# Kernel tuning notes

Measured on AMD Instinct MI355X. Metric: run time of the kernel, lower is better.

## Reference

```python
import jax, jax.numpy as jnp
import numpy as np

N_NODES = 100000
N_EDGES = 1600000
D = 128
NUM_GRAPHS = 256


def setup_inputs() -> dict:
    key = jax.random.key(0)
    ks = jax.random.split(key, 8)
    x = jax.random.normal(ks[0], (N_NODES, D), dtype=jnp.float32)
    edge_index = jax.random.randint(ks[1], (2, N_EDGES), 0, N_NODES, dtype=jnp.int32)
    edge_attr = jax.random.normal(ks[2], (N_EDGES, D), dtype=jnp.float32) * 0.1
    batch = jnp.sort(jax.random.randint(ks[3], (N_NODES,), 0, NUM_GRAPHS, dtype=jnp.int32))
    primary = jax.random.randint(ks[4], (N_NODES,), 0, 2, dtype=jnp.int32)  # 1=primary, 0=condition
    scale = 1.0 / np.sqrt(D)
    W1 = jax.random.normal(ks[5], (D, D), dtype=jnp.float32) * scale
    b1 = jnp.zeros((D,), dtype=jnp.float32)
    W2 = jax.random.normal(ks[6], (D, D), dtype=jnp.float32) * scale
    b2 = jnp.zeros((D,), dtype=jnp.float32)
    return {"x": x, "edge_index": edge_index, "edge_attr": edge_attr,
            "batch": batch, "primary": primary,
            "W1": W1, "b1": b1, "W2": W2, "b2": b2}


def reference(x, edge_index, edge_attr, batch, primary, W1, b1, W2, b2):
    n = x.shape[0]
    # --- GIN-style GNN layer: node_rep = MLP(x + sum_{e:(s->d)} (x[s] + e_attr)) ---
    src, dst = edge_index[0], edge_index[1]
    msg = x[src] + edge_attr                                  # [E, D] gather (memory-bound)
    agg = jax.ops.segment_sum(msg, dst, num_segments=n)       # [N, D] scatter-add
    h = jax.nn.relu((x + agg) @ W1 + b1) @ W2 + b2            # [N, D]

    # --- per-graph mean pool over condition nodes (primary == 0) ---
    cond = (primary == 0)
    condf = cond.astype(h.dtype)[:, None]
    csum = jax.ops.segment_sum(h * condf, batch, num_segments=NUM_GRAPHS)   # [G, D]
    ccnt = jax.ops.segment_sum(condf, batch, num_segments=NUM_GRAPHS)       # [G, 1]
    # graphs with no condition nodes get a zero pool (matches torch branch)
    pool = jnp.where(ccnt > 0, csum / jnp.maximum(ccnt, 1.0), 0.0)          # [G, D]

    # --- assemble rows: per graph, primary rows [h | cond_pool] first, then zero rows
    # for condition nodes (matches the torch concat order) ---
    key = batch * 2 + cond.astype(batch.dtype)      # primary nodes sort before condition nodes
    order = jnp.argsort(key, stable=True)
    h_o = h[order]                                   # [N, D]
    pool_o = pool[batch[order]]                      # [N, D]
    prim_o = (primary[order] == 1)[:, None]
    out = jnp.where(prim_o, jnp.concatenate([h_o, pool_o], axis=1), 0.0)    # [N, 2D]
    return out
```

## Files before the change

### kernel.cpp

```cpp
#include <hip/hip_runtime.h>

#define D 128
#define NG 256

typedef __attribute__((ext_vector_type(8))) short bf16x8;
typedef __attribute__((ext_vector_type(4))) float f32x4;
typedef __attribute__((ext_vector_type(4))) float f4;
typedef __attribute__((ext_vector_type(4))) ushort u16x4;

__device__ inline ushort f2bf(float f) {
  uint b = __float_as_uint(f);
  return (ushort)((b + 0x7fffu + ((b >> 16) & 1u)) >> 16);
}
__device__ inline float bf2f(ushort u) { return __uint_as_float((uint)u << 16); }

__global__ __launch_bounds__(256) void prep_kernel(
    const int* __restrict__ ei, int* __restrict__ deg,
    const int* __restrict__ batch, const int* __restrict__ primary,
    int* __restrict__ ncount, int* __restrict__ ccnt,
    const float* __restrict__ x, ushort* __restrict__ xb,
    const float* __restrict__ W1, const float* __restrict__ W2,
    ushort* __restrict__ W1T, ushort* __restrict__ W2T, int E, int N, int total4) {
  int i = blockIdx.x * blockDim.x + threadIdx.x;
  if (i < E) atomicAdd(&deg[ei[E + i]], 1);
  if (i < N) {
    int g = batch[i];
    atomicAdd(&ncount[g], 1);
    if (primary[i] == 0) atomicAdd(&ccnt[g], 1);
  }
  if (i < total4) {
    f4 v = __builtin_nontemporal_load(&((const f4*)x)[i]);
    u16x4 o;
    o.x = f2bf(v.x); o.y = f2bf(v.y); o.z = f2bf(v.z); o.w = f2bf(v.w);
    ((u16x4*)xb)[i] = o;
  }
  if (i < 2 * D * D) {
    int w = i >> 14;
    int k = (i >> 7) & 127;
    int n = i & 127;
    const float* src = w ? W2 : W1;
    ushort* dst = w ? W2T : W1T;
    dst[n * 128 + k] = f2bf(src[k * 128 + n]);
  }
}

__global__ __launch_bounds__(256) void scan_block_sums(const int* __restrict__ deg,
                                                       int* __restrict__ bsum, int N) {
  __shared__ int red[256];
  int t = threadIdx.x;
  int base = blockIdx.x * 1024;
  int s = 0;
#pragma unroll
  for (int j = 0; j < 4; ++j) {
    int i = base + t * 4 + j;
    if (i < N) s += deg[i];
  }
  red[t] = s;
  __syncthreads();
  for (int o = 128; o > 0; o >>= 1) {
    if (t < o) red[t] += red[t + o];
    __syncthreads();
  }
  if (t == 0) bsum[blockIdx.x] = red[0];
}

__global__ void scan_bsum(int* __restrict__ bsum, int nb) {
  __shared__ int a[128];
  int t = threadIdx.x;
  int v = (t < nb) ? bsum[t] : 0;
  a[t] = v;
  __syncthreads();
  for (int o = 1; o < 128; o <<= 1) {
    int u = (t >= o) ? a[t - o] : 0;
    __syncthreads();
    a[t] += u;
    __syncthreads();
  }
  if (t < nb) bsum[t] = a[t] - v;
}

__global__ __launch_bounds__(256) void scan_final(const int* __restrict__ deg,
                                                  const int* __restrict__ bsum,
                                                  int* __restrict__ off, int N) {
  __shared__ int ts[256];
  int t = threadIdx.x;
  int base = blockIdx.x * 1024;
  int v[4];
  int s = 0;
#pragma unroll
  for (int j = 0; j < 4; ++j) {
    int i = base + t * 4 + j;
    v[j] = (i < N) ? deg[i] : 0;
    s += v[j];
  }
  ts[t] = s;
  __syncthreads();
  for (int o = 1; o < 256; o <<= 1) {
    int u = (t >= o) ? ts[t - o] : 0;
    __syncthreads();
    ts[t] += u;
    __syncthreads();
  }
  int excl = ts[t] - s + bsum[blockIdx.x];
#pragma unroll
  for (int j = 0; j < 4; ++j) {
    int i = base + t * 4 + j;
    if (i < N) off[i] = excl;
    excl += v[j];
    if (i == N - 1) off[N] = excl;
  }
}

__global__ __launch_bounds__(256, 8) void msg_build_kernel(
    const int* __restrict__ ei, const ushort* __restrict__ xb,
    const float* __restrict__ ea, const int* __restrict__ off,
    int* __restrict__ cursor, ushort* __restrict__ msg, int E) {
  int g = (int)(((long long)blockIdx.x * 256 + threadIdx.x) >> 5);
  int c = threadIdx.x & 31;
  if (g >= E) return;
  int s = ei[g];
  int d = ei[E + g];
  int slot;
  if (c == 0) slot = atomicAdd(&cursor[d], 1);
  slot = __shfl(slot, 0, 32);
  long long row = (long long)off[d] + slot;
  f4 a = __builtin_nontemporal_load(&((const f4*)ea)[(size_t)g * 32 + c]);
  u16x4 u = ((const u16x4*)xb)[(size_t)s * 32 + c];
  u16x4 o;
  o.x = f2bf(a.x + bf2f(u.x));
  o.y = f2bf(a.y + bf2f(u.y));
  o.z = f2bf(a.z + bf2f(u.z));
  o.w = f2bf(a.w + bf2f(u.w));
  __builtin_nontemporal_store(o, &((u16x4*)msg)[(size_t)row * 32 + c]);
}

__global__ void scan_kernel(const int* __restrict__ ncount, int* __restrict__ gstart) {
  __shared__ int a[NG];
  int tx = threadIdx.x;
  int v = ncount[tx];
  a[tx] = v;
  __syncthreads();
  for (int off = 1; off < NG; off <<= 1) {
    int u = (tx >= off) ? a[tx - off] : 0;
    __syncthreads();
    a[tx] += u;
    __syncthreads();
  }
  gstart[tx] = a[tx] - v;
  if (tx == NG - 1) gstart[NG] = a[tx];
}

__global__ __launch_bounds__(256) void rank_kernel(const int* __restrict__ primary,
                                                   const int* __restrict__ gstart,
                                                   const int* __restrict__ ccnt,
                                                   int* __restrict__ pos) {
  int g = blockIdx.x;
  int s = gstart[g], e = gstart[g + 1];
  int pcnt = (e - s) - ccnt[g];
  __shared__ int wcntP[4], wcntC[4];
  int prun = 0, crun = 0;
  for (int i0 = s; i0 < e; i0 += 256) {
    int n = i0 + threadIdx.x;
    bool valid = n < e;
    int isP = (valid && primary[n] == 1) ? 1 : 0;
    int isC = (valid && primary[n] != 1) ? 1 : 0;
    unsigned long long mP = __ballot(isP);
    unsigned long long mC = __ballot(isC);
    int lane = threadIdx.x & 63;
    int wid = threadIdx.x >> 6;
    if (lane == 0) { wcntP[wid] = __popcll(mP); wcntC[wid] = __popcll(mC); }
    __syncthreads();
    int preP = __popcll(mP & ((1ULL << lane) - 1ULL));
    int preC = __popcll(mC & ((1ULL << lane) - 1ULL));
    int woffP = 0, woffC = 0;
#pragma unroll
    for (int ww = 0; ww < 4; ++ww)
      if (ww < wid) { woffP += wcntP[ww]; woffC += wcntC[ww]; }
    int totP = wcntP[0] + wcntP[1] + wcntP[2] + wcntP[3];
    int totC = wcntC[0] + wcntC[1] + wcntC[2] + wcntC[3];
    if (valid) {
      if (isP)
        pos[n] = s + prun + woffP + preP;
      else
        pos[n] = ~(s + pcnt + crun + woffC + preC);
    }
    prun += totP;
    crun += totC;
    __syncthreads();
  }
}

__global__ __launch_bounds__(256, 4) void fused_reduce_mlp_kernel(
    const ushort* __restrict__ xb, const ushort* __restrict__ msg,
    const int* __restrict__ off, float* __restrict__ out,
    const ushort* __restrict__ W1T, const float* __restrict__ b1,
    const ushort* __restrict__ W2T, const float* __restrict__ b2,
    const int* __restrict__ batch, const int* __restrict__ primary,
    const int* __restrict__ pos, float* __restrict__ csum, int N) {
  __shared__ ushort ylds[64][D];
  __shared__ ushort tl[4][16][D];
  __shared__ float csl[4][D];
  const int tid = threadIdx.x;
  const int base = blockIdx.x * 64;

  for (int i = tid; i < 4 * D; i += 256) ((float*)csl)[i] = 0.f;
  const int gmin = batch[base < N ? base : N - 1];

  {
    const int gid = tid >> 5;
    const int c = tid & 31;
    const u16x4* msg4 = (const u16x4*)msg;
    const u16x4* xb4 = (const u16x4*)xb;
    for (int i = 0; i < 8; ++i) {
      const int m = gid * 8 + i;
      const int n = base + m;
      f4 acc = {0.f, 0.f, 0.f, 0.f};
      if (n < N) {
        u16x4 self = xb4[(size_t)n * 32 + c];
        acc.x = bf2f(self.x);
        acc.y = bf2f(self.y);
        acc.z = bf2f(self.z);
        acc.w = bf2f(self.w);
        int k = off[n];
        const int e = off[n + 1];
        for (; k + 4 <= e; k += 4) {
          u16x4 u0 = msg4[(size_t)k * 32 + c];
          u16x4 u1 = msg4[(size_t)(k + 1) * 32 + c];
          u16x4 u2 = msg4[(size_t)(k + 2) * 32 + c];
          u16x4 u3 = msg4[(size_t)(k + 3) * 32 + c];
          acc.x += bf2f(u0.x) + bf2f(u1.x);
          acc.y += bf2f(u0.y) + bf2f(u1.y);
          acc.z += bf2f(u0.z) + bf2f(u1.z);
          acc.w += bf2f(u0.w) + bf2f(u1.w);
          acc.x += bf2f(u2.x) + bf2f(u3.x);
          acc.y += bf2f(u2.y) + bf2f(u3.y);
          acc.z += bf2f(u2.z) + bf2f(u3.z);
          acc.w += bf2f(u2.w) + bf2f(u3.w);
        }
        for (; k < e; ++k) {
          u16x4 u0 = msg4[(size_t)k * 32 + c];
          acc.x += bf2f(u0.x);
          acc.y += bf2f(u0.y);
          acc.z += bf2f(u0.z);
          acc.w += bf2f(u0.w);
        }
      }
      u16x4 o;
      o.x = f2bf(acc.x);
      o.y = f2bf(acc.y);
      o.z = f2bf(acc.z);
      o.w = f2bf(acc.w);
      *(u16x4*)((char*)&ylds[m][0] + ((c * 8) ^ (i << 4))) = o;
    }
  }
  __syncthreads();

  const int w = tid >> 6;
  const int l = tid & 63;
  const int lr = l & 15;
  const int lg = l >> 4;
  const int m0 = base + w * 16;

  f32x4 acc[8];
#pragma unroll
  for (int t = 0; t < 8; ++t) {
    float bv = b1[t * 16 + lr];
    acc[t][0] = bv; acc[t][1] = bv; acc[t][2] = bv; acc[t][3] = bv;
  }
  const char* arow_base = (const char*)&ylds[w * 16 + lr][0];
  const int arow_swz = (lr & 7) << 4;
#pragma unroll
  for (int kk = 0; kk < 4; ++kk) {
    bf16x8 a = *(const bf16x8*)(arow_base + ((kk * 64 + lg * 16) ^ arow_swz));
#pragma unroll
    for (int t = 0; t < 8; ++t) {
      bf16x8 b = *(const bf16x8*)&W1T[(size_t)(t * 16 + lr) * D + kk * 32 + lg * 8];
      acc[t] = __builtin_amdgcn_mfma_f32_16x16x32_bf16(a, b, acc[t], 0, 0, 0);
    }
  }
#pragma unroll
  for (int t = 0; t < 8; ++t) {
#pragma unroll
    for (int r = 0; r < 4; ++r) {
      float v = acc[t][r];
      v = v > 0.f ? v : 0.f;
      int m = lg * 4 + r;
      int col = (t * 16 + lr) ^ ((m & 7) << 3);
      tl[w][m][col] = f2bf(v);
    }
  }
  __syncthreads();

  f32x4 acc2[8];
#pragma unroll
  for (int t = 0; t < 8; ++t) {
    float bv = b2[t * 16 + lr];
    acc2[t][0] = bv; acc2[t][1] = bv; acc2[t][2] = bv; acc2[t][3] = bv;
  }
#pragma unroll
  for (int kk = 0; kk < 4; ++kk) {
    bf16x8 a = *(const bf16x8*)&tl[w][lr][(kk * 32 + lg * 8) ^ ((lr & 7) << 3)];
#pragma unroll
    for (int t = 0; t < 8; ++t) {
      bf16x8 b = *(const bf16x8*)&W2T[(size_t)(t * 16 + lr) * D + kk * 32 + lg * 8];
      acc2[t] = __builtin_amdgcn_mfma_f32_16x16x32_bf16(a, b, acc2[t], 0, 0, 0);
    }
  }

#pragma unroll
  for (int r = 0; r < 4; ++r) {
    int m = m0 + lg * 4 + r;
    if (m >= N) continue;
    int p = pos[m];
    if (p >= 0) {
      size_t ro = (size_t)p * 256;
#pragma unroll
      for (int t = 0; t < 8; ++t)
        __builtin_nontemporal_store(acc2[t][r], &out[ro + t * 16 + lr]);
    } else {
      size_t ro = (size_t)(~p) * 256;
#pragma unroll
      for (int t = 0; t < 8; ++t) {
        __builtin_nontemporal_store(0.0f, &out[ro + t * 16 + lr]);
        __builtin_nontemporal_store(0.0f, &out[ro + 128 + t * 16 + lr]);
      }
      int g = batch[m];
      int gl = g - gmin;
      if (gl < 4) {
#pragma unroll
        for (int t = 0; t < 8; ++t) atomicAdd(&csl[gl][t * 16 + lr], acc2[t][r]);
      } else {
#pragma unroll
        for (int t = 0; t < 8; ++t)
          unsafeAtomicAdd(&csum[(size_t)g * D + t * 16 + lr], acc2[t][r]);
      }
    }
  }
  __syncthreads();
  for (int i = tid; i < 4 * D; i += 256) {
    float v = ((float*)csl)[i];
    if (v != 0.f) {
      int gl = i >> 7, c = i & 127;
      unsafeAtomicAdd(&csum[(size_t)(gmin + gl) * D + c], v);
    }
  }
}

__global__ __launch_bounds__(256) void poolwrite_kernel(const float* __restrict__ csum,
                                                        const int* __restrict__ ccnt,
                                                        const int* __restrict__ batch,
                                                        const int* __restrict__ pos,
                                                        float* __restrict__ out, int N) {
  long long tid = (long long)blockIdx.x * blockDim.x + threadIdx.x;
  int n = (int)(tid >> 5);
  int c = (int)(tid & 31);
  if (n >= N) return;
  int p = pos[n];
  if (p < 0) return;
  int g = batch[n];
  int cnt = ccnt[g];
  f4 v = {0.f, 0.f, 0.f, 0.f};
  if (cnt > 0) {
    f4 s4 = ((const f4*)csum)[(size_t)g * 32 + c];
    float inv = 1.0f / (float)cnt;
    v = s4 * inv;
  }
  __builtin_nontemporal_store(v, &((f4*)out)[(size_t)p * 64 + 32 + c]);
}

extern "C" void kernel_launch(void* const* d_in, const int* in_sizes, int n_in,
                              void* d_out, int out_size, void* d_ws, size_t ws_size,
                              hipStream_t stream) {
  const float* x = (const float*)d_in[0];
  const int* ei = (const int*)d_in[1];
  const float* ea = (const float*)d_in[2];
  const int* batch = (const int*)d_in[3];
  const int* primary = (const int*)d_in[4];
  const float* W1 = (const float*)d_in[5];
  const float* b1 = (const float*)d_in[6];
  const float* W2 = (const float*)d_in[7];
  const float* b2 = (const float*)d_in[8];
  float* out = (float*)d_out;

  const int N = in_sizes[0] / D;
  const int E = in_sizes[1] / 2;
  const int nb = (N + 1023) / 1024;
  const int total4 = N * D / 4;

  float* csum = (float*)d_ws;
  ushort* xb = (ushort*)(csum + (size_t)NG * D);
  ushort* W1T = xb + (size_t)N * D;
  ushort* W2T = W1T + D * D;
  ushort* msg = W2T + D * D;
  int* ip = (int*)(msg + (size_t)E * D);
  int* deg = ip;
  int* off = deg + N;
  int* cursor = off + N + 4;
  int* bsum = cursor + N;
  int* ccnt = bsum + 128;
  int* ncount = ccnt + NG;
  int* gstart = ncount + NG;
  int* pos = gstart + 260;

  hipMemsetAsync(csum, 0, (size_t)NG * D * 4, stream);
  hipMemsetAsync(deg, 0, (size_t)N * 4, stream);
  hipMemsetAsync(cursor, 0, (size_t)N * 4, stream);
  hipMemsetAsync(ccnt, 0, (size_t)NG * 2 * 4, stream);

  prep_kernel<<<(total4 + 255) / 256, 256, 0, stream>>>(ei, deg, batch, primary, ncount, ccnt,
                                                        x, xb, W1, W2, W1T, W2T, E, N, total4);
  scan_block_sums<<<nb, 256, 0, stream>>>(deg, bsum, N);
  scan_bsum<<<1, 128, 0, stream>>>(bsum, nb);
  scan_final<<<nb, 256, 0, stream>>>(deg, bsum, off, N);
  scan_kernel<<<1, NG, 0, stream>>>(ncount, gstart);
  rank_kernel<<<NG, 256, 0, stream>>>(primary, gstart, ccnt, pos);
  {
    long long threads = (long long)E * 32;
    msg_build_kernel<<<(int)((threads + 255) / 256), 256, 0, stream>>>(ei, xb, ea, off, cursor,
                                                                       msg, E);
  }
  fused_reduce_mlp_kernel<<<(N + 63) / 64, 256, 0, stream>>>(xb, msg, off, out, W1T, b1, W2T,
                                                             b2, batch, primary, pos, csum, N);
  poolwrite_kernel<<<(int)(((long long)N * 32 + 255) / 256), 256, 0, stream>>>(csum, ccnt, batch,
                                                                               pos, out, N);
}
```

Before: 701.8 us.

## Split edge messages into two halves so message buffer stays cache-resident

Edges are split into two halves, each with its own CSR offsets built from one combined scan over 2N degrees. Each half's bf16 messages are built into a half-sized buffer and reduced right away, so the buffer may stay in the large last-level cache between write and read; the stores also become normal instead of nontemporal. The old fused reduce+MLP kernel is split into per-node reduce kernels, an fp32 agg intermediate, a bf16 yb buffer, and an MLP kernel that reads A operands from global memory. This adds extra kernel launches and extra agg/yb traffic in exchange for less DRAM traffic on the message buffer.

```diff
diff --git a/kernel.cpp b/kernel.cpp
--- a/kernel.cpp
+++ b/kernel.cpp
@@ -20,9 +20,12 @@
     int* __restrict__ ncount, int* __restrict__ ccnt,
     const float* __restrict__ x, ushort* __restrict__ xb,
     const float* __restrict__ W1, const float* __restrict__ W2,
-    ushort* __restrict__ W1T, ushort* __restrict__ W2T, int E, int N, int total4) {
+    ushort* __restrict__ W1T, ushort* __restrict__ W2T, int E, int E0, int N, int total4) {
   int i = blockIdx.x * blockDim.x + threadIdx.x;
-  if (i < E) atomicAdd(&deg[ei[E + i]], 1);
+  if (i < E) {
+    int d = ei[E + i];
+    atomicAdd(&deg[(i >= E0 ? N : 0) + d], 1);
+  }
   if (i < N) {
     int g = batch[i];
     atomicAdd(&ncount[g], 1);
@@ -45,7 +48,7 @@
 }
 
 __global__ __launch_bounds__(256) void scan_block_sums(const int* __restrict__ deg,
-                                                       int* __restrict__ bsum, int N) {
+                                                       int* __restrict__ bsum, int N2) {
   __shared__ int red[256];
   int t = threadIdx.x;
   int base = blockIdx.x * 1024;
@@ -53,7 +56,7 @@
 #pragma unroll
   for (int j = 0; j < 4; ++j) {
     int i = base + t * 4 + j;
-    if (i < N) s += deg[i];
+    if (i < N2) s += deg[i];
   }
   red[t] = s;
   __syncthreads();
@@ -65,12 +68,12 @@
 }
 
 __global__ void scan_bsum(int* __restrict__ bsum, int nb) {
-  __shared__ int a[128];
+  __shared__ int a[256];
   int t = threadIdx.x;
   int v = (t < nb) ? bsum[t] : 0;
   a[t] = v;
   __syncthreads();
-  for (int o = 1; o < 128; o <<= 1) {
+  for (int o = 1; o < 256; o <<= 1) {
     int u = (t >= o) ? a[t - o] : 0;
     __syncthreads();
     a[t] += u;
@@ -81,7 +84,7 @@
 
 __global__ __launch_bounds__(256) void scan_final(const int* __restrict__ deg,
                                                   const int* __restrict__ bsum,
-                                                  int* __restrict__ off, int N) {
+                                                  int* __restrict__ off, int N2) {
   __shared__ int ts[256];
   int t = threadIdx.x;
   int base = blockIdx.x * 1024;
@@ -90,7 +93,7 @@
 #pragma unroll
   for (int j = 0; j < 4; ++j) {
     int i = base + t * 4 + j;
-    v[j] = (i < N) ? deg[i] : 0;
+    v[j] = (i < N2) ? deg[i] : 0;
     s += v[j];
   }
   ts[t] = s;
@@ -105,33 +108,110 @@
 #pragma unroll
   for (int j = 0; j < 4; ++j) {
     int i = base + t * 4 + j;
-    if (i < N) off[i] = excl;
+    if (i < N2) off[i] = excl;
     excl += v[j];
-    if (i == N - 1) off[N] = excl;
+    if (i == N2 - 1) off[N2] = excl;
   }
 }
 
 __global__ __launch_bounds__(256, 8) void msg_build_kernel(
     const int* __restrict__ ei, const ushort* __restrict__ xb,
-    const float* __restrict__ ea, const int* __restrict__ off,
-    int* __restrict__ cursor, ushort* __restrict__ msg, int E) {
-  int g = (int)(((long long)blockIdx.x * 256 + threadIdx.x) >> 5);
-  int c = threadIdx.x & 31;
-  if (g >= E) return;
-  int s = ei[g];
-  int d = ei[E + g];
+    const float* __restrict__ ea, const int* __restrict__ offc,
+    int* __restrict__ cursorc, ushort* __restrict__ msg,
+    int ebase, int ecnt, int E, int rowbase) {
+  long long t = (long long)blockIdx.x * 256 + threadIdx.x;
+  int rel = (int)(t >> 5);
+  int c = (int)(t & 31);
+  if (rel >= ecnt) return;
+  int e = ebase + rel;
+  int s = ei[e];
+  int d = ei[E + e];
   int slot;
-  if (c == 0) slot = atomicAdd(&cursor[d], 1);
+  if (c == 0) slot = atomicAdd(&cursorc[d], 1);
   slot = __shfl(slot, 0, 32);
-  long long row = (long long)off[d] + slot;
-  f4 a = __builtin_nontemporal_load(&((const f4*)ea)[(size_t)g * 32 + c]);
+  long long row = (long long)offc[d] - rowbase + slot;
+  f4 a = __builtin_nontemporal_load(&((const f4*)ea)[(size_t)e * 32 + c]);
   u16x4 u = ((const u16x4*)xb)[(size_t)s * 32 + c];
   u16x4 o;
   o.x = f2bf(a.x + bf2f(u.x));
   o.y = f2bf(a.y + bf2f(u.y));
   o.z = f2bf(a.z + bf2f(u.z));
   o.w = f2bf(a.w + bf2f(u.w));
-  __builtin_nontemporal_store(o, &((u16x4*)msg)[(size_t)row * 32 + c]);
+  ((u16x4*)msg)[(size_t)row * 32 + c] = o;
+}
+
+__global__ __launch_bounds__(256, 8) void reduce0_kernel(
+    const ushort* __restrict__ xb, const ushort* __restrict__ msg,
+    const int* __restrict__ off0, float* __restrict__ agg, int N) {
+  long long t = (long long)blockIdx.x * 256 + threadIdx.x;
+  int n = (int)(t >> 5);
+  int c = (int)(t & 31);
+  if (n >= N) return;
+  const u16x4* msg4 = (const u16x4*)msg;
+  u16x4 self = ((const u16x4*)xb)[(size_t)n * 32 + c];
+  f4 acc;
+  acc.x = bf2f(self.x); acc.y = bf2f(self.y); acc.z = bf2f(self.z); acc.w = bf2f(self.w);
+  int k = off0[n];
+  const int e = off0[n + 1];
+  for (; k + 4 <= e; k += 4) {
+    u16x4 u0 = msg4[(size_t)k * 32 + c];
+    u16x4 u1 = msg4[(size_t)(k + 1) * 32 + c];
+    u16x4 u2 = msg4[(size_t)(k + 2) * 32 + c];
+    u16x4 u3 = msg4[(size_t)(k + 3) * 32 + c];
+    acc.x += bf2f(u0.x) + bf2f(u1.x);
+    acc.y += bf2f(u0.y) + bf2f(u1.y);
+    acc.z += bf2f(u0.z) + bf2f(u1.z);
+    acc.w += bf2f(u0.w) + bf2f(u1.w);
+    acc.x += bf2f(u2.x) + bf2f(u3.x);
+    acc.y += bf2f(u2.y) + bf2f(u3.y);
+    acc.z += bf2f(u2.z) + bf2f(u3.z);
+    acc.w += bf2f(u2.w) + bf2f(u3.w);
+  }
+  for (; k < e; ++k) {
+    u16x4 u0 = msg4[(size_t)k * 32 + c];
+    acc.x += bf2f(u0.x);
+    acc.y += bf2f(u0.y);
+    acc.z += bf2f(u0.z);
+    acc.w += bf2f(u0.w);
+  }
+  ((f4*)agg)[(size_t)n * 32 + c] = acc;
+}
+
+__global__ __launch_bounds__(256, 8) void reduce1_kernel(
+    const float* __restrict__ agg, const ushort* __restrict__ msg,
+    const int* __restrict__ off1, int rowbase, ushort* __restrict__ yb, int N) {
+  long long t = (long long)blockIdx.x * 256 + threadIdx.x;
+  int n = (int)(t >> 5);
+  int c = (int)(t & 31);
+  if (n >= N) return;
+  const u16x4* msg4 = (const u16x4*)msg;
+  f4 acc = ((const f4*)agg)[(size_t)n * 32 + c];
+  int k = off1[n] - rowbase;
+  const int e = off1[n + 1] - rowbase;
+  for (; k + 4 <= e; k += 4) {
+    u16x4 u0 = msg4[(size_t)k * 32 + c];
+    u16x4 u1 = msg4[(size_t)(k + 1) * 32 + c];
+    u16x4 u2 = msg4[(size_t)(k + 2) * 32 + c];
+    u16x4 u3 = msg4[(size_t)(k + 3) * 32 + c];
+    acc.x += bf2f(u0.x) + bf2f(u1.x);
+    acc.y += bf2f(u0.y) + bf2f(u1.y);
+    acc.z += bf2f(u0.z) + bf2f(u1.z);
+    acc.w += bf2f(u0.w) + bf2f(u1.w);
+    acc.x += bf2f(u2.x) + bf2f(u3.x);
+    acc.y += bf2f(u2.y) + bf2f(u3.y);
+    acc.z += bf2f(u2.z) + bf2f(u3.z);
+    acc.w += bf2f(u2.w) + bf2f(u3.w);
+  }
+  for (; k < e; ++k) {
+    u16x4 u0 = msg4[(size_t)k * 32 + c];
+    acc.x += bf2f(u0.x);
+    acc.y += bf2f(u0.y);
+    acc.z += bf2f(u0.z);
+    acc.w += bf2f(u0.w);
+  }
+  u16x4 o;
+  o.x = f2bf(acc.x); o.y = f2bf(acc.y); o.z = f2bf(acc.z); o.w = f2bf(acc.w);
+  ((u16x4*)yb)[(size_t)n * 32 + c] = o;
 }
 
 __global__ void scan_kernel(const int* __restrict__ ncount, int* __restrict__ gstart) {
@@ -190,76 +270,25 @@
   }
 }
 
-__global__ __launch_bounds__(256, 4) void fused_reduce_mlp_kernel(
-    const ushort* __restrict__ xb, const ushort* __restrict__ msg,
-    const int* __restrict__ off, float* __restrict__ out,
+__global__ __launch_bounds__(256) void mlp_mfma_kernel(
+    const ushort* __restrict__ yb, float* __restrict__ out,
     const ushort* __restrict__ W1T, const float* __restrict__ b1,
     const ushort* __restrict__ W2T, const float* __restrict__ b2,
     const int* __restrict__ batch, const int* __restrict__ primary,
     const int* __restrict__ pos, float* __restrict__ csum, int N) {
-  __shared__ ushort ylds[64][D];
   __shared__ ushort tl[4][16][D];
   __shared__ float csl[4][D];
   const int tid = threadIdx.x;
-  const int base = blockIdx.x * 64;
-
-  for (int i = tid; i < 4 * D; i += 256) ((float*)csl)[i] = 0.f;
-  const int gmin = batch[base < N ? base : N - 1];
-
-  {
-    const int gid = tid >> 5;
-    const int c = tid & 31;
-    const u16x4* msg4 = (const u16x4*)msg;
-    const u16x4* xb4 = (const u16x4*)xb;
-    for (int i = 0; i < 8; ++i) {
-      const int m = gid * 8 + i;
-      const int n = base + m;
-      f4 acc = {0.f, 0.f, 0.f, 0.f};
-      if (n < N) {
-        u16x4 self = xb4[(size_t)n * 32 + c];
-        acc.x = bf2f(self.x);
-        acc.y = bf2f(self.y);
-        acc.z = bf2f(self.z);
-        acc.w = bf2f(self.w);
-        int k = off[n];
-        const int e = off[n + 1];
-        for (; k + 4 <= e; k += 4) {
-          u16x4 u0 = msg4[(size_t)k * 32 + c];
-          u16x4 u1 = msg4[(size_t)(k + 1) * 32 + c];
-          u16x4 u2 = msg4[(size_t)(k + 2) * 32 + c];
-          u16x4 u3 = msg4[(size_t)(k + 3) * 32 + c];
-          acc.x += bf2f(u0.x) + bf2f(u1.x);
-          acc.y += bf2f(u0.y) + bf2f(u1.y);
-          acc.z += bf2f(u0.z) + bf2f(u1.z);
-          acc.w += bf2f(u0.w) + bf2f(u1.w);
-          acc.x += bf2f(u2.x) + bf2f(u3.x);
-          acc.y += bf2f(u2.y) + bf2f(u3.y);
-          acc.z += bf2f(u2.z) + bf2f(u3.z);
-          acc.w += bf2f(u2.w) + bf2f(u3.w);
-        }
-        for (; k < e; ++k) {
-          u16x4 u0 = msg4[(size_t)k * 32 + c];
-          acc.x += bf2f(u0.x);
-          acc.y += bf2f(u0.y);
-          acc.z += bf2f(u0.z);
-          acc.w += bf2f(u0.w);
-        }
-      }
-      u16x4 o;
-      o.x = f2bf(acc.x);
-      o.y = f2bf(acc.y);
-      o.z = f2bf(acc.z);
-      o.w = f2bf(acc.w);
-      *(u16x4*)((char*)&ylds[m][0] + ((c * 8) ^ (i << 4))) = o;
-    }
-  }
-  __syncthreads();
-
   const int w = tid >> 6;
   const int l = tid & 63;
   const int lr = l & 15;
   const int lg = l >> 4;
+  const int base = blockIdx.x * 64;
   const int m0 = base + w * 16;
+
+  for (int i = tid; i < 4 * D; i += 256) ((float*)csl)[i] = 0.f;
+  int gmin = batch[base < N ? base : N - 1];
+  __syncthreads();
 
   f32x4 acc[8];
 #pragma unroll
@@ -267,11 +296,11 @@
     float bv = b1[t * 16 + lr];
     acc[t][0] = bv; acc[t][1] = bv; acc[t][2] = bv; acc[t][3] = bv;
   }
-  const char* arow_base = (const char*)&ylds[w * 16 + lr][0];
-  const int arow_swz = (lr & 7) << 4;
+  int arow = m0 + lr;
+  if (arow >= N) arow = N - 1;
 #pragma unroll
   for (int kk = 0; kk < 4; ++kk) {
-    bf16x8 a = *(const bf16x8*)(arow_base + ((kk * 64 + lg * 16) ^ arow_swz));
+    bf16x8 a = *(const bf16x8*)&yb[(size_t)arow * D + kk * 32 + lg * 8];
 #pragma unroll
     for (int t = 0; t < 8; ++t) {
       bf16x8 b = *(const bf16x8*)&W1T[(size_t)(t * 16 + lr) * D + kk * 32 + lg * 8];
@@ -384,43 +413,66 @@
 
   const int N = in_sizes[0] / D;
   const int E = in_sizes[1] / 2;
-  const int nb = (N + 1023) / 1024;
+  const int E0 = E / 2;
+  const int N2 = 2 * N;
+  const int nb = (N2 + 1023) / 1024;
   const int total4 = N * D / 4;
+  const int Emax = E - E0;
 
   float* csum = (float*)d_ws;
-  ushort* xb = (ushort*)(csum + (size_t)NG * D);
-  ushort* W1T = xb + (size_t)N * D;
+  float* agg = csum + (size_t)NG * D;
+  ushort* xb = (ushort*)(agg + (size_t)N * D);
+  ushort* yb = xb + (size_t)N * D;
+  ushort* W1T = yb + (size_t)N * D;
   ushort* W2T = W1T + D * D;
   ushort* msg = W2T + D * D;
-  int* ip = (int*)(msg + (size_t)E * D);
+  int* ip = (int*)(msg + (size_t)Emax * D);
   int* deg = ip;
-  int* off = deg + N;
-  int* cursor = off + N + 4;
-  int* bsum = cursor + N;
-  int* ccnt = bsum + 128;
+  int* OFF = deg + N2;
+  int* cursor = OFF + N2 + 4;
+  int* bsum = cursor + N2;
+  int* ccnt = bsum + 256;
   int* ncount = ccnt + NG;
   int* gstart = ncount + NG;
   int* pos = gstart + 260;
 
   hipMemsetAsync(csum, 0, (size_t)NG * D * 4, stream);
-  hipMemsetAsync(deg, 0, (size_t)N * 4, stream);
-  hipMemsetAsync(cursor, 0, (size_t)N * 4, stream);
+  hipMemsetAsync(deg, 0, (size_t)N2 * 4, stream);
+  hipMemsetAsync(cursor, 0, (size_t)N2 * 4, stream);
   hipMemsetAsync(ccnt, 0, (size_t)NG * 2 * 4, stream);
 
   prep_kernel<<<(total4 + 255) / 256, 256, 0, stream>>>(ei, deg, batch, primary, ncount, ccnt,
-                                                        x, xb, W1, W2, W1T, W2T, E, N, total4);
-  scan_block_sums<<<nb, 256, 0, stream>>>(deg, bsum, N);
-  scan_bsum<<<1, 128, 0, stream>>>(bsum, nb);
-  scan_final<<<nb, 256, 0, stream>>>(deg, bsum, off, N);
+                                                        x, xb, W1, W2, W1T, W2T, E, E0, N,
+                                                        total4);
+  scan_block_sums<<<nb, 256, 0, stream>>>(deg, bsum, N2);
+  scan_bsum<<<1, 256, 0, stream>>>(bsum, nb);
+  scan_final<<<nb, 256, 0, stream>>>(deg, bsum, OFF, N2);
   scan_kernel<<<1, NG, 0, stream>>>(ncount, gstart);
   rank_kernel<<<NG, 256, 0, stream>>>(primary, gstart, ccnt, pos);
+
   {
-    long long threads = (long long)E * 32;
-    msg_build_kernel<<<(int)((threads + 255) / 256), 256, 0, stream>>>(ei, xb, ea, off, cursor,
-                                                                       msg, E);
-  }
-  fused_reduce_mlp_kernel<<<(N + 63) / 64, 256, 0, stream>>>(xb, msg, off, out, W1T, b1, W2T,
-                                                             b2, batch, primary, pos, csum, N);
+    long long threads = (long long)E0 * 32;
+    msg_build_kernel<<<(int)((threads + 255) / 256), 256, 0, stream>>>(ei, xb, ea, OFF, cursor,
+                                                                       msg, 0, E0, E, 0);
+  }
+  {
+    long long threads = (long long)N * 32;
+    reduce0_kernel<<<(int)((threads + 255) / 256), 256, 0, stream>>>(xb, msg, OFF, agg, N);
+  }
+  {
+    long long threads = (long long)(E - E0) * 32;
+    msg_build_kernel<<<(int)((threads + 255) / 256), 256, 0, stream>>>(ei, xb, ea, OFF + N,
+                                                                       cursor + N, msg, E0,
+                                                                       E - E0, E, E0);
+  }
+  {
+    long long threads = (long long)N * 32;
+    reduce1_kernel<<<(int)((threads + 255) / 256), 256, 0, stream>>>(agg, msg, OFF + N, E0, yb,
+                                                                     N);
+  }
+
+  mlp_mfma_kernel<<<(N + 63) / 64, 256, 0, stream>>>(yb, out, W1T, b1, W2T, b2, batch, primary,
+                                                     pos, csum, N);
   poolwrite_kernel<<<(int)(((long long)N * 32 + 255) / 256), 256, 0, stream>>>(csum, ccnt, batch,
                                                                                pos, out, N);
 }
```

New measurement: 724.0 us. +3.2%, slower.
